# Kernel optimization log

Measured on AMD Instinct MI355X. Metric: run time of the kernel, lower is better.

## Reference

```python
import jax, jax.numpy as jnp
import numpy as np

H = 16        # query heads
KV = 4        # key/value heads
HD = 64       # head dim
BASE = 10000.0
SCALE = HD ** (-0.5) * 0.8


def setup_inputs() -> dict:
    key = jax.random.key(0)
    ks = jax.random.split(key, 5)
    B, S, D = 2, 4096, 1024
    return {
        "hidden_states": jax.random.normal(ks[0], (B, S, D), dtype=jnp.float32),
        "wq": jax.random.normal(ks[1], (D, H * HD), dtype=jnp.float32) * (D ** -0.5),
        "wk": jax.random.normal(ks[2], (D, KV * HD), dtype=jnp.float32) * (D ** -0.5),
        "wv": jax.random.normal(ks[3], (D, KV * HD), dtype=jnp.float32) * (D ** -0.5),
        "wo": jax.random.normal(ks[4], (H * HD, D), dtype=jnp.float32) * ((H * HD) ** -0.5),
    }


def _rope_tables(seq_len, dtype):
    inv_freq = 1.0 / (BASE ** (jnp.arange(0, HD, 2, dtype=jnp.float32) / HD))
    t = jnp.arange(seq_len, dtype=jnp.float32)
    freqs = t[:, None] * inv_freq[None, :]            # [S, HD/2]
    emb = jnp.concatenate([freqs, freqs], axis=-1)    # [S, HD]
    return jnp.cos(emb).astype(dtype), jnp.sin(emb).astype(dtype)


def _rotate_half(x):
    x1, x2 = x[..., : HD // 2], x[..., HD // 2 :]
    return jnp.concatenate([-x2, x1], axis=-1)


def reference(hidden_states, wq, wk, wv, wo):
    B, S, D = hidden_states.shape
    G = H // KV
    q = (hidden_states @ wq).reshape(B, S, H, HD).transpose(0, 2, 1, 3)   # [B,H,S,HD]
    k = (hidden_states @ wk).reshape(B, S, KV, HD).transpose(0, 2, 1, 3)  # [B,KV,S,HD]
    v = (hidden_states @ wv).reshape(B, S, KV, HD).transpose(0, 2, 1, 3)
    cos, sin = _rope_tables(S, q.dtype)               # [S,HD] each
    cos = cos[None, None]                             # [1,1,S,HD]
    sin = sin[None, None]
    q = q * cos + _rotate_half(q) * sin
    k = k * cos + _rotate_half(k) * sin
    k = jnp.repeat(k, G, axis=1)                      # [B,H,S,HD]
    v = jnp.repeat(v, G, axis=1)
    scores = jnp.einsum("bhqd,bhkd->bhqk", q, k) * SCALE
    probs = jax.nn.softmax(scores.astype(jnp.float32), axis=-1).astype(q.dtype)
    out = jnp.einsum("bhqk,bhkd->bhqd", probs, v)     # [B,H,S,HD]
    out = out.transpose(0, 2, 1, 3).reshape(B, S, H * HD)
    return out @ wo
```

## Files before the change

### kernel.cpp

```cpp
#include <hip/hip_runtime.h>
#include <hip/hip_fp16.h>
#include <math.h>

typedef _Float16 f16;
typedef _Float16 half8 __attribute__((ext_vector_type(8)));
typedef _Float16 half4v __attribute__((ext_vector_type(4)));
typedef _Float16 half2v __attribute__((ext_vector_type(2)));
typedef float f32x4 __attribute__((ext_vector_type(4)));
typedef float f32x16 __attribute__((ext_vector_type(16)));
typedef unsigned uint2v __attribute__((ext_vector_type(2)));

#define NB 2
#define NS 4096
#define ND 1024
#define NH 16
#define NKV 4
#define NHD 64
#define ATT_SCALE2 0.14426950408889634f

__global__ __launch_bounds__(256) void wprep_k(
    const float* __restrict__ wq, const float* __restrict__ wk,
    const float* __restrict__ wv, const float* __restrict__ wo,
    f16* __restrict__ Bt, f16* __restrict__ Wot, float* __restrict__ ropet)
{
  __shared__ f16 tile[64][72];
  int bx = blockIdx.x, by = blockIdx.y;
  int tid = threadIdx.x;
  if (bx >= 40) {
    int e0 = (((bx - 40) * 16 + by) * 256 + tid) * 4;
    #pragma unroll
    for (int i = 0; i < 4; ++i) {
      int e = e0 + i;
      int s = e >> 5, d = e & 31;
      double inv = exp((double)d * -0.28782313662425575);
      double ang = (double)s * inv;
      ropet[e]          = (float)cos(ang);
      ropet[131072 + e] = (float)sin(ang);
    }
    return;
  }
  const float* src; int ldn, colbase, nbase; f16* dst;
  if (bx < 24) {
    int n0 = bx * 64;
    if (n0 < 1024)      { src = wq; ldn = 1024; colbase = n0; }
    else if (n0 < 1280) { src = wk; ldn = 256;  colbase = n0 - 1024; }
    else                { src = wv; ldn = 256;  colbase = n0 - 1280; }
    dst = Bt; nbase = n0;
  } else {
    src = wo; ldn = 1024; colbase = (bx - 24) * 64; dst = Wot; nbase = (bx - 24) * 64;
  }
  int kr = tid >> 4;
  int nc = (tid & 15) * 4;
  #pragma unroll
  for (int i = 0; i < 4; ++i) {
    int k = by * 64 + kr + i * 16;
    float4 v = *reinterpret_cast<const float4*>(src + (size_t)k * ldn + colbase + nc);
    tile[nc + 0][kr + i * 16] = (f16)v.x;
    tile[nc + 1][kr + i * 16] = (f16)v.y;
    tile[nc + 2][kr + i * 16] = (f16)v.z;
    tile[nc + 3][kr + i * 16] = (f16)v.w;
  }
  __syncthreads();
  int nl = tid >> 2;
  int kb = (tid & 3) * 16;
  half8 a = *reinterpret_cast<const half8*>(&tile[nl][kb]);
  half8 b = *reinterpret_cast<const half8*>(&tile[nl][kb + 8]);
  f16* o = dst + (size_t)(nbase + nl) * 1024 + by * 64 + kb;
  *reinterpret_cast<half8*>(o) = a;
  *reinterpret_cast<half8*>(o + 8) = b;
}

template<int MODE>
__global__ __launch_bounds__(256) void gemm_k(
    const float* __restrict__ Af32, const f16* __restrict__ Af16,
    const f16* __restrict__ Bt, const float* __restrict__ ropet,
    f16* __restrict__ q_h, f16* __restrict__ k_h, f16* __restrict__ vT_h,
    float* __restrict__ outp)
{
  __shared__ f16 As[128 * 32];
  __shared__ f16 Bs[128 * 32];
  int tid = threadIdx.x;
  int lane = tid & 63, w = tid >> 6;
  int wr = w >> 1, wc = w & 1;
  int g = lane >> 4, lr = lane & 15;
  int m0 = blockIdx.y * 128, n0 = blockIdx.x * 128;

  f32x4 acc[4][4] = {};

  int ar = tid >> 1;
  int ac = (tid & 1) * 16;

  for (int k0 = 0; k0 < ND; k0 += 32) {
    if (MODE == 0) {
      const float* Ap = Af32 + (size_t)(m0 + ar) * ND + k0 + ac;
      #pragma unroll
      for (int i = 0; i < 4; ++i) {
        float4 v = *reinterpret_cast<const float4*>(Ap + i * 4);
        int col = ac + i * 4;
        int slot = (col >> 3) ^ (ar & 3);
        half4v hv = { (f16)v.x, (f16)v.y, (f16)v.z, (f16)v.w };
        *reinterpret_cast<half4v*>(&As[ar * 32 + slot * 8 + (col & 7)]) = hv;
      }
    } else {
      const f16* Ap = Af16 + (size_t)(m0 + ar) * ND + k0 + ac;
      half8 v0 = *reinterpret_cast<const half8*>(Ap);
      half8 v1 = *reinterpret_cast<const half8*>(Ap + 8);
      int s0 = (ac >> 3) ^ (ar & 3);
      int s1 = ((ac >> 3) + 1) ^ (ar & 3);
      *reinterpret_cast<half8*>(&As[ar * 32 + s0 * 8]) = v0;
      *reinterpret_cast<half8*>(&As[ar * 32 + s1 * 8]) = v1;
    }
    {
      const f16* Bp = Bt + (size_t)(n0 + ar) * ND + k0 + ac;
      half8 v0 = *reinterpret_cast<const half8*>(Bp);
      half8 v1 = *reinterpret_cast<const half8*>(Bp + 8);
      int s0 = (ac >> 3) ^ (ar & 3);
      int s1 = ((ac >> 3) + 1) ^ (ar & 3);
      *reinterpret_cast<half8*>(&Bs[ar * 32 + s0 * 8]) = v0;
      *reinterpret_cast<half8*>(&Bs[ar * 32 + s1 * 8]) = v1;
    }
    __syncthreads();
    half8 af[4], bf[4];
    #pragma unroll
    for (int mt = 0; mt < 4; ++mt) {
      int row = wr * 64 + mt * 16 + lr;
      af[mt] = *reinterpret_cast<const half8*>(&As[row * 32 + (g ^ (row & 3)) * 8]);
    }
    #pragma unroll
    for (int nt = 0; nt < 4; ++nt) {
      int row = wc * 64 + nt * 16 + lr;
      bf[nt] = *reinterpret_cast<const half8*>(&Bs[row * 32 + (g ^ (row & 3)) * 8]);
    }
    #pragma unroll
    for (int mt = 0; mt < 4; ++mt)
      #pragma unroll
      for (int nt = 0; nt < 4; ++nt)
        acc[mt][nt] = __builtin_amdgcn_mfma_f32_16x16x32_f16(af[mt], bf[nt], acc[mt][nt], 0, 0, 0);
    __syncthreads();
  }

  if (MODE == 0) {
    #pragma unroll
    for (int mt = 0; mt < 4; ++mt)
      #pragma unroll
      for (int r = 0; r < 4; ++r) {
        int m = m0 + wr * 64 + mt * 16 + g * 4 + r;
        int b = m >> 12, s = m & (NS - 1);
        #pragma unroll
        for (int nt = 0; nt < 2; ++nt) {
          int n_lo = n0 + wc * 64 + nt * 16 + lr;
          float x1 = acc[mt][nt][r];
          float x2 = acc[mt][nt + 2][r];
          if (n_lo < 1280) {
            int d = nt * 16 + lr;
            float c  = ropet[s * 32 + d];
            float si = ropet[131072 + s * 32 + d];
            f16 o1 = (f16)(x1 * c - x2 * si);
            f16 o2 = (f16)(x2 * c + x1 * si);
            if (n_lo < 1024) {
              f16* qp = q_h + (((size_t)b * NH + (n_lo >> 6)) * NS + s) * NHD + d;
              qp[0] = o1; qp[32] = o2;
            } else {
              int nn = n_lo - 1024;
              f16* kp = k_h + (((size_t)b * NKV + (nn >> 6)) * NS + s) * NHD + d;
              kp[0] = o1; kp[32] = o2;
            }
          } else {
            int nn = n_lo - 1280;
            f16* vp = vT_h + (((size_t)b * NKV + (nn >> 6)) * NHD + (nn & 63)) * NS + s;
            vp[0] = (f16)x1;
            vp[32 * NS] = (f16)x2;
          }
        }
      }
  } else {
    #pragma unroll
    for (int mt = 0; mt < 4; ++mt)
      #pragma unroll
      for (int nt = 0; nt < 4; ++nt)
        #pragma unroll
        for (int r = 0; r < 4; ++r) {
          int m = m0 + wr * 64 + mt * 16 + g * 4 + r;
          int n = n0 + wc * 64 + nt * 16 + lr;
          outp[(size_t)m * ND + n] = acc[mt][nt][r];
        }
  }
}

__global__ __launch_bounds__(512) void attn_k(
    const f16* __restrict__ q_h, const f16* __restrict__ k_h,
    const f16* __restrict__ vT_h, f16* __restrict__ attn_h)
{
  __shared__ f16 Ks[2][64 * 64];
  __shared__ f16 Vs[2][64 * 64];
  int tid = threadIdx.x;
  int lane = tid & 63, w = tid >> 6;
  int hi = lane >> 5, qr = lane & 31;
  int bh = blockIdx.x; int b = bh >> 4, h = bh & 15, kvh = h >> 2;
  int q0 = blockIdx.y * 256 + w * 32;

  const f16* qptr = q_h + (((size_t)b * NH + h) * NS + q0 + qr) * NHD + hi * 8;
  half8 qf[4];
  #pragma unroll
  for (int ks = 0; ks < 4; ++ks)
    qf[ks] = *reinterpret_cast<const half8*>(qptr + 16 * ks);

  const f16* kbase = k_h + ((size_t)b * NKV + kvh) * NS * NHD;
  const f16* vbase = vT_h + ((size_t)b * NKV + kvh) * NHD * NS;

  f32x16 accO[2] = {};
  float m_run = 0.0f;
  float l_lane = 0.f;

  int srow = tid >> 3;
  int scol = (tid & 7) * 8;
  int sslot = ((scol >> 3) ^ (srow & 7)) * 8;
  int qs = qr & 7;

  {
    half8 kv0 = *reinterpret_cast<const half8*>(kbase + (size_t)srow * NHD + scol);
    half8 vv0 = *reinterpret_cast<const half8*>(vbase + (size_t)srow * NS + scol);
    *reinterpret_cast<half8*>(&Ks[0][srow * 64 + sslot]) = kv0;
    *reinterpret_cast<half8*>(&Vs[0][srow * 64 + sslot]) = vv0;
  }

  const half2v ones2 = { (f16)1.0f, (f16)1.0f };

  unsigned wrd[2][4][2];

#define SMCHUNK(KB, SC, E, LACC) do { \
    float a0_ = exp2f(fmaf((SC)[(E) * 4 + 0], ATT_SCALE2, -m_run)); \
    float a1_ = exp2f(fmaf((SC)[(E) * 4 + 1], ATT_SCALE2, -m_run)); \
    unsigned u0_ = __builtin_bit_cast(unsigned, __builtin_amdgcn_cvt_pkrtz(a0_, a1_)); \
    wrd[KB][E][0] = u0_; \
    LACC = __builtin_amdgcn_fdot2(__builtin_bit_cast(half2v, u0_), ones2, LACC, false); \
    float a2_ = exp2f(fmaf((SC)[(E) * 4 + 2], ATT_SCALE2, -m_run)); \
    float a3_ = exp2f(fmaf((SC)[(E) * 4 + 3], ATT_SCALE2, -m_run)); \
    unsigned u1_ = __builtin_bit_cast(unsigned, __builtin_amdgcn_cvt_pkrtz(a2_, a3_)); \
    wrd[KB][E][1] = u1_; \
    LACC = __builtin_amdgcn_fdot2(__builtin_bit_cast(half2v, u1_), ones2, LACC, false); \
  } while (0)

#define QK1STEP(KS) do { \
    int cs_ = 2 * (KS) + hi; \
    half8 kf1_ = *reinterpret_cast<const half8*>(&Kc[(32 + qr) * 64 + ((cs_ ^ qs) << 3)]); \
    __builtin_amdgcn_s_setprio(1); \
    sc1 = __builtin_amdgcn_mfma_f32_32x32x16_f16(kf1_, qf[KS], sc1, 0, 0, 0); \
    __builtin_amdgcn_s_setprio(0); \
  } while (0)

#define PVSTEP(KS) do { \
    int kb_ = (KS) >> 1, e0_ = 2 * ((KS) & 1); \
    uint2v s0_ = __builtin_amdgcn_permlane32_swap(wrd[kb_][e0_][0], wrd[kb_][e0_ + 1][0], false, false); \
    uint2v s1_ = __builtin_amdgcn_permlane32_swap(wrd[kb_][e0_][1], wrd[kb_][e0_ + 1][1], false, false); \
    union { unsigned u[4]; half8 h; } pfu_; \
    pfu_.u[0] = s0_[0]; pfu_.u[1] = s1_[0]; pfu_.u[2] = s0_[1]; pfu_.u[3] = s1_[1]; \
    int cs_ = 2 * (KS) + hi; \
    half8 vf0_ = *reinterpret_cast<const half8*>(&Vc[qr * 64 + ((cs_ ^ qs) << 3)]); \
    half8 vf1_ = *reinterpret_cast<const half8*>(&Vc[(32 + qr) * 64 + ((cs_ ^ qs) << 3)]); \
    __builtin_amdgcn_s_setprio(1); \
    accO[0] = __builtin_amdgcn_mfma_f32_32x32x16_f16(vf0_, pfu_.h, accO[0], 0, 0, 0); \
    accO[1] = __builtin_amdgcn_mfma_f32_32x32x16_f16(vf1_, pfu_.h, accO[1], 0, 0, 0); \
    __builtin_amdgcn_s_setprio(0); \
  } while (0)

  int cur = 0;
  for (int t = 0; t < 64; ++t) {
    __syncthreads();
    int tn = (t < 63) ? t + 1 : t;
    int kt2 = tn * 64;
    half8 kreg = *reinterpret_cast<const half8*>(kbase + (size_t)(kt2 + srow) * NHD + scol);
    half8 vreg = *reinterpret_cast<const half8*>(vbase + (size_t)srow * NS + kt2 + scol);

    const f16* Kc = &Ks[cur][0];
    const f16* Vc = &Vs[cur][0];

    f32x16 sc0 = {}, sc1 = {};
    #pragma unroll
    for (int ks = 0; ks < 4; ++ks) {
      int cs = 2 * ks + hi;
      half8 kf0 = *reinterpret_cast<const half8*>(&Kc[qr * 64 + ((cs ^ qs) << 3)]);
      __builtin_amdgcn_s_setprio(1);
      sc0 = __builtin_amdgcn_mfma_f32_32x32x16_f16(kf0, qf[ks], sc0, 0, 0, 0);
      __builtin_amdgcn_s_setprio(0);
    }

    float l0 = 0.f, l1 = 0.f;
    QK1STEP(0); SMCHUNK(0, sc0, 0, l0);
    QK1STEP(1); SMCHUNK(0, sc0, 1, l0);
    QK1STEP(2); SMCHUNK(0, sc0, 2, l0);
    QK1STEP(3); SMCHUNK(0, sc0, 3, l0);

    PVSTEP(0);  SMCHUNK(1, sc1, 0, l1);
    PVSTEP(1);  SMCHUNK(1, sc1, 1, l1);
    PVSTEP(2);  SMCHUNK(1, sc1, 2, l1);
    SMCHUNK(1, sc1, 3, l1);
    PVSTEP(3);

    float ltile = l0 + l1;
    l_lane += ltile;

    if (__any(ltile > 16384.0f)) {
      const float alpha = 0x1p-16f;
      #pragma unroll
      for (int db = 0; db < 2; ++db)
        #pragma unroll
        for (int i = 0; i < 16; ++i) accO[db][i] *= alpha;
      l_lane *= alpha;
      m_run += 16.0f;
    }

    *reinterpret_cast<half8*>(&Ks[cur ^ 1][srow * 64 + sslot]) = kreg;
    *reinterpret_cast<half8*>(&Vs[cur ^ 1][srow * 64 + sslot]) = vreg;
    cur ^= 1;
  }
#undef SMCHUNK
#undef QK1STEP
#undef PVSTEP

  float l_tot = l_lane + __shfl_xor(l_lane, 32);
  float inv_l = 1.0f / l_tot;
  f16* obase = attn_h + ((size_t)b * NS + q0 + qr) * ND + h * NHD;
  #pragma unroll
  for (int db = 0; db < 2; ++db)
    #pragma unroll
    for (int e = 0; e < 4; ++e) {
      half4v ov = { (f16)(accO[db][e * 4 + 0] * inv_l), (f16)(accO[db][e * 4 + 1] * inv_l),
                    (f16)(accO[db][e * 4 + 2] * inv_l), (f16)(accO[db][e * 4 + 3] * inv_l) };
      *reinterpret_cast<half4v*>(obase + db * 32 + e * 8 + hi * 4) = ov;
    }
}

extern "C" void kernel_launch(void* const* d_in, const int* in_sizes, int n_in,
                              void* d_out, int out_size, void* d_ws, size_t ws_size,
                              hipStream_t stream)
{
  (void)in_sizes; (void)n_in; (void)out_size; (void)ws_size;
  const float* hs = (const float*)d_in[0];
  const float* wq = (const float*)d_in[1];
  const float* wk = (const float*)d_in[2];
  const float* wv = (const float*)d_in[3];
  const float* wo = (const float*)d_in[4];
  float* outp = (float*)d_out;

  f16* q_h    = (f16*)d_ws;
  f16* k_h    = q_h    + (size_t)NB * NH * NS * NHD;
  f16* vT_h   = k_h    + (size_t)NB * NKV * NS * NHD;
  f16* attn_h = vT_h   + (size_t)NB * NKV * NS * NHD;
  f16* Bt     = attn_h + (size_t)NB * NS * ND;
  f16* Wot    = Bt     + (size_t)1536 * 1024;
  float* ropet = (float*)attn_h;

  wprep_k<<<dim3(48, 16), 256, 0, stream>>>(wq, wk, wv, wo, Bt, Wot, ropet);
  gemm_k<0><<<dim3(12, 64), 256, 0, stream>>>(hs, nullptr, Bt, ropet, q_h, k_h, vT_h, nullptr);
  attn_k<<<dim3(32, 16), 512, 0, stream>>>(q_h, k_h, vT_h, attn_h);
  gemm_k<1><<<dim3(8, 64), 256, 0, stream>>>(nullptr, attn_h, Wot, nullptr, nullptr, nullptr, nullptr, outp);
}
```

Baseline: 315.4 us.

## Double-buffer GEMM LDS tiles with async global-to-LDS loads

Converts the projection GEMM main loop to a double-buffered LDS scheme. The next K-slice of B (and of A in f16 mode) is prefetched with global_load_lds directly into the alternate buffer, and f32 A is loaded into registers early and converted after the MFMAs. This cuts the loop to one barrier per iteration and overlaps global loads with compute. In exchange it doubles LDS use, and correctness depends on the async LDS loads completing before the next barrier (vmcnt waits).

New measurement: 354.4 us. 1.12x slower.

```diff
diff --git a/kernel.cpp b/kernel.cpp
--- a/kernel.cpp
+++ b/kernel.cpp
@@ -17,6 +17,10 @@
 #define NKV 4
 #define NHD 64
 #define ATT_SCALE2 0.14426950408889634f
+
+#define GL16(gp, lp) __builtin_amdgcn_global_load_lds( \
+    (const __attribute__((address_space(1))) unsigned int*)(const void*)(gp), \
+    (__attribute__((address_space(3))) unsigned int*)(void*)(lp), 16, 0, 0)
 
 __global__ __launch_bounds__(256) void wprep_k(
     const float* __restrict__ wq, const float* __restrict__ wk,
@@ -77,8 +81,8 @@
     f16* __restrict__ q_h, f16* __restrict__ k_h, f16* __restrict__ vT_h,
     float* __restrict__ outp)
 {
-  __shared__ f16 As[128 * 32];
-  __shared__ f16 Bs[128 * 32];
+  __shared__ f16 As[2][128 * 32];
+  __shared__ f16 Bs[2][128 * 32];
   int tid = threadIdx.x;
   int lane = tid & 63, w = tid >> 6;
   int wr = w >> 1, wc = w & 1;
@@ -87,56 +91,81 @@
 
   f32x4 acc[4][4] = {};
 
+  int srow = w * 16 + (lane >> 2);
+  int scol8 = (lane & 3) ^ ((lane >> 2) & 3);
   int ar = tid >> 1;
   int ac = (tid & 1) * 16;
 
-  for (int k0 = 0; k0 < ND; k0 += 32) {
+  {
+    const f16* Bp = Bt + (size_t)(n0 + srow) * ND + scol8 * 8;
+    GL16(Bp,                   (char*)&Bs[0][0] + w * 1024);
+    GL16(Bp + (size_t)64 * ND, (char*)&Bs[0][0] + 4096 + w * 1024);
     if (MODE == 0) {
-      const float* Ap = Af32 + (size_t)(m0 + ar) * ND + k0 + ac;
+      const float* Ap = Af32 + (size_t)(m0 + ar) * ND + ac;
       #pragma unroll
       for (int i = 0; i < 4; ++i) {
         float4 v = *reinterpret_cast<const float4*>(Ap + i * 4);
         int col = ac + i * 4;
         int slot = (col >> 3) ^ (ar & 3);
         half4v hv = { (f16)v.x, (f16)v.y, (f16)v.z, (f16)v.w };
-        *reinterpret_cast<half4v*>(&As[ar * 32 + slot * 8 + (col & 7)]) = hv;
+        *reinterpret_cast<half4v*>(&As[0][ar * 32 + slot * 8 + (col & 7)]) = hv;
       }
     } else {
-      const f16* Ap = Af16 + (size_t)(m0 + ar) * ND + k0 + ac;
-      half8 v0 = *reinterpret_cast<const half8*>(Ap);
-      half8 v1 = *reinterpret_cast<const half8*>(Ap + 8);
-      int s0 = (ac >> 3) ^ (ar & 3);
-      int s1 = ((ac >> 3) + 1) ^ (ar & 3);
-      *reinterpret_cast<half8*>(&As[ar * 32 + s0 * 8]) = v0;
-      *reinterpret_cast<half8*>(&As[ar * 32 + s1 * 8]) = v1;
-    }
-    {
-      const f16* Bp = Bt + (size_t)(n0 + ar) * ND + k0 + ac;
-      half8 v0 = *reinterpret_cast<const half8*>(Bp);
-      half8 v1 = *reinterpret_cast<const half8*>(Bp + 8);
-      int s0 = (ac >> 3) ^ (ar & 3);
-      int s1 = ((ac >> 3) + 1) ^ (ar & 3);
-      *reinterpret_cast<half8*>(&Bs[ar * 32 + s0 * 8]) = v0;
-      *reinterpret_cast<half8*>(&Bs[ar * 32 + s1 * 8]) = v1;
-    }
+      const f16* Ap = Af16 + (size_t)(m0 + srow) * ND + scol8 * 8;
+      GL16(Ap,                   (char*)&As[0][0] + w * 1024);
+      GL16(Ap + (size_t)64 * ND, (char*)&As[0][0] + 4096 + w * 1024);
+    }
+  }
+
+  for (int k0 = 0; k0 < ND; k0 += 32) {
+    int cur = (k0 >> 5) & 1;
     __syncthreads();
+
+    float4 apre[4];
+    bool more = (k0 + 32 < ND);
+    if (more) {
+      int kn = k0 + 32;
+      const f16* Bp = Bt + (size_t)(n0 + srow) * ND + kn + scol8 * 8;
+      GL16(Bp,                   (char*)&Bs[cur ^ 1][0] + w * 1024);
+      GL16(Bp + (size_t)64 * ND, (char*)&Bs[cur ^ 1][0] + 4096 + w * 1024);
+      if (MODE == 0) {
+        const float* Ap = Af32 + (size_t)(m0 + ar) * ND + kn + ac;
+        #pragma unroll
+        for (int i = 0; i < 4; ++i)
+          apre[i] = *reinterpret_cast<const float4*>(Ap + i * 4);
+      } else {
+        const f16* Ap = Af16 + (size_t)(m0 + srow) * ND + kn + scol8 * 8;
+        GL16(Ap,                   (char*)&As[cur ^ 1][0] + w * 1024);
+        GL16(Ap + (size_t)64 * ND, (char*)&As[cur ^ 1][0] + 4096 + w * 1024);
+      }
+    }
+
     half8 af[4], bf[4];
     #pragma unroll
     for (int mt = 0; mt < 4; ++mt) {
       int row = wr * 64 + mt * 16 + lr;
-      af[mt] = *reinterpret_cast<const half8*>(&As[row * 32 + (g ^ (row & 3)) * 8]);
+      af[mt] = *reinterpret_cast<const half8*>(&As[cur][row * 32 + (g ^ (row & 3)) * 8]);
     }
     #pragma unroll
     for (int nt = 0; nt < 4; ++nt) {
       int row = wc * 64 + nt * 16 + lr;
-      bf[nt] = *reinterpret_cast<const half8*>(&Bs[row * 32 + (g ^ (row & 3)) * 8]);
+      bf[nt] = *reinterpret_cast<const half8*>(&Bs[cur][row * 32 + (g ^ (row & 3)) * 8]);
     }
     #pragma unroll
     for (int mt = 0; mt < 4; ++mt)
       #pragma unroll
       for (int nt = 0; nt < 4; ++nt)
         acc[mt][nt] = __builtin_amdgcn_mfma_f32_16x16x32_f16(af[mt], bf[nt], acc[mt][nt], 0, 0, 0);
-    __syncthreads();
+
+    if (MODE == 0 && more) {
+      #pragma unroll
+      for (int i = 0; i < 4; ++i) {
+        int col = ac + i * 4;
+        int slot = (col >> 3) ^ (ar & 3);
+        half4v hv = { (f16)apre[i].x, (f16)apre[i].y, (f16)apre[i].z, (f16)apre[i].w };
+        *reinterpret_cast<half4v*>(&As[cur ^ 1][ar * 32 + slot * 8 + (col & 7)]) = hv;
+      }
+    }
   }
 
   if (MODE == 0) {
```
